# Kernel optimization log

Hardware: AMD Instinct MI355X
Metric: run time of the kernel (lower is better)

The kernel has to match this reference:

```python
import jax, jax.numpy as jnp
import numpy as np

B, H, W, C = 8, 112, 112, 128
NH, WS, SR, HIDDEN = 4, 7, 8, 512
EPS = 1e-5

def ln(x, g, b):
    mu = jnp.mean(x, axis=-1, keepdims=True)
    var = jnp.var(x, axis=-1, keepdims=True)
    return (x - mu) * jax.lax.rsqrt(var + EPS) * g + b

def local_attn(x, qkv_w, qkv_b, pw, pb):
    # windowed attention: (H,W) tiled into WSxWS windows, H%WS==W%WS==0 so no pad
    Bx, N, Cx = x.shape
    hd = Cx // NH
    _h, _w = H // WS, W // WS
    xw = x.reshape(Bx, _h, WS, _w, WS, Cx).transpose(0, 1, 3, 2, 4, 5)
    xw = xw.reshape(Bx, _h * _w, WS * WS, Cx)
    qkv = (xw @ qkv_w + qkv_b).reshape(Bx, _h * _w, WS * WS, 3, NH, hd)
    qkv = qkv.transpose(3, 0, 1, 4, 2, 5)  # 3, B, nW, NH, ws2, hd
    q, k, v = qkv[0], qkv[1], qkv[2]
    attn = jax.nn.softmax((q @ jnp.swapaxes(k, -2, -1)) * (hd ** -0.5), axis=-1)
    o = (attn @ v).transpose(0, 1, 3, 2, 4).reshape(Bx, _h, _w, WS, WS, Cx)
    o = o.transpose(0, 1, 3, 2, 4, 5).reshape(Bx, N, Cx)
    return o @ pw + pb

def global_attn(x, qw, qb, kvw, kvb, srw, srb, sng, snb, pw, pb):
    Bx, N, Cx = x.shape
    hd = Cx // NH
    q = (x @ qw + qb).reshape(Bx, N, NH, hd).transpose(0, 2, 1, 3)  # B,NH,N,hd
    xi = x.reshape(Bx, H, W, Cx)
    xs = jax.lax.conv_general_dilated(xi, srw, (SR, SR), 'VALID',
                                      dimension_numbers=('NHWC', 'HWIO', 'NHWC')) + srb
    xs = ln(xs.reshape(Bx, -1, Cx), sng, snb)  # B, M, C  (M = (H/SR)*(W/SR))
    kv = (xs @ kvw + kvb).reshape(Bx, -1, 2, NH, hd)
    k = kv[:, :, 0].transpose(0, 2, 1, 3)
    v = kv[:, :, 1].transpose(0, 2, 1, 3)
    attn = jax.nn.softmax(jnp.einsum('bhnd,bhmd->bhnm', q, k) * (hd ** -0.5), axis=-1)
    o = jnp.einsum('bhnm,bhmd->bhnd', attn, v).transpose(0, 2, 1, 3).reshape(Bx, N, Cx)
    return o @ pw + pb

def mlp(x, f1w, f1b, dww, dwb, f2w, f2b):
    h = x @ f1w + f1b
    hi = h.reshape(x.shape[0], H, W, HIDDEN)
    hi = jax.lax.conv_general_dilated(hi, dww, (1, 1), 'SAME',
                                      dimension_numbers=('NHWC', 'HWIO', 'NHWC'),
                                      feature_group_count=HIDDEN) + dwb
    h = jax.nn.gelu(hi.reshape(x.shape[0], -1, HIDDEN), approximate=False)
    return h @ f2w + f2b

def reference(x, l_n1_g, l_n1_b, l_qkv_w, l_qkv_b, l_pw, l_pb, l_n2_g, l_n2_b,
              l_f1w, l_f1b, l_dww, l_dwb, l_f2w, l_f2b,
              g_n1_g, g_n1_b, g_qw, g_qb, g_kvw, g_kvb, g_srw, g_srb, g_sng, g_snb,
              g_pw, g_pb, g_n2_g, g_n2_b, g_f1w, g_f1b, g_dww, g_dwb, g_f2w, g_f2b):
    # Local-attention Block
    x = x + local_attn(ln(x, l_n1_g, l_n1_b), l_qkv_w, l_qkv_b, l_pw, l_pb)
    x = x + mlp(ln(x, l_n2_g, l_n2_b), l_f1w, l_f1b, l_dww, l_dwb, l_f2w, l_f2b)
    # Global (spatial-reduction) attention Block
    x = x + global_attn(ln(x, g_n1_g, g_n1_b), g_qw, g_qb, g_kvw, g_kvb,
                        g_srw, g_srb, g_sng, g_snb, g_pw, g_pb)
    x = x + mlp(ln(x, g_n2_g, g_n2_b), g_f1w, g_f1b, g_dww, g_dwb, g_f2w, g_f2b)
    return x

def setup_inputs() -> dict:
    key = jax.random.key(0)
    cnt = [0]
    def rn(shp, s=0.02):
        cnt[0] += 1
        return (jax.random.normal(jax.random.fold_in(key, cnt[0]), shp, dtype=jnp.float32) * s)
    z = lambda shp: jnp.zeros(shp, jnp.float32)
    o = lambda shp: jnp.ones(shp, jnp.float32)
    return {
        'x': rn((B, H * W, C), 1.0),
        'l_n1_g': o((C,)), 'l_n1_b': z((C,)),
        'l_qkv_w': rn((C, 3 * C)), 'l_qkv_b': z((3 * C,)),
        'l_pw': rn((C, C)), 'l_pb': z((C,)),
        'l_n2_g': o((C,)), 'l_n2_b': z((C,)),
        'l_f1w': rn((C, HIDDEN)), 'l_f1b': z((HIDDEN,)),
        'l_dww': rn((3, 3, 1, HIDDEN), 0.1), 'l_dwb': z((HIDDEN,)),
        'l_f2w': rn((HIDDEN, C)), 'l_f2b': z((C,)),
        'g_n1_g': o((C,)), 'g_n1_b': z((C,)),
        'g_qw': rn((C, C)), 'g_qb': z((C,)),
        'g_kvw': rn((C, 2 * C)), 'g_kvb': z((2 * C,)),
        'g_srw': rn((SR, SR, C, C), 0.02), 'g_srb': z((C,)),
        'g_sng': o((C,)), 'g_snb': z((C,)),
        'g_pw': rn((C, C)), 'g_pb': z((C,)),
        'g_n2_g': o((C,)), 'g_n2_b': z((C,)),
        'g_f1w': rn((C, HIDDEN)), 'g_f1b': z((HIDDEN,)),
        'g_dww': rn((3, 3, 1, HIDDEN), 0.1), 'g_dwb': z((HIDDEN,)),
        'g_f2w': rn((HIDDEN, C)), 'g_f2b': z((C,)),
    }
```

## Files before the change

kernel.cpp:

```cpp
#include <hip/hip_runtime.h>
#include <hip/hip_bf16.h>

#define DI __device__ __forceinline__

typedef __attribute__((ext_vector_type(8))) __bf16 bf16x8;
typedef __attribute__((ext_vector_type(8))) short short8;
typedef __attribute__((ext_vector_type(4))) short short4v;
typedef __attribute__((ext_vector_type(4))) float f32x4;

DI short f2b(float f) {
    union { float f; unsigned u; } v; v.f = f;
    unsigned r = v.u + 0x7FFFu + ((v.u >> 16) & 1u);
    return (short)(r >> 16);
}
DI float b2f(short s) {
    union { unsigned u; float f; } v; v.u = ((unsigned)(unsigned short)s) << 16;
    return v.f;
}

DI void gll16(const short* g, short* l) {
    __builtin_amdgcn_global_load_lds(
        (const __attribute__((address_space(1))) void*)(g),
        (__attribute__((address_space(3))) void*)(l), 16, 0, 0);
}

DI float gelu(float a) {
    float z = fabsf(a) * 0.7071067811865475f;
    float t = __builtin_amdgcn_rcpf(fmaf(0.3275911f, z, 1.f));
    float p = t * fmaf(t, fmaf(t, fmaf(t, fmaf(t, 1.061405429f, -1.453152027f),
                                       1.421413741f), -0.284496736f), 0.254829592f);
    float e = __expf(-z * z);
    float er = fmaf(-p, e, 1.f);
    float sg = (a >= 0.f) ? er : -er;
    return 0.5f * a * (1.f + sg);
}

template<int OB, int HB, int HR, int LNO>
__global__ __launch_bounds__(256)
void gemm128(const short* __restrict__ A, int lda,
             const short* __restrict__ Wt, int ldw,
             const float* __restrict__ bias,
             void* __restrict__ Cv, int ldc,
             const float* __restrict__ R, int ldr,
             const float* __restrict__ lng, const float* __restrict__ lnb,
             short* __restrict__ lnout,
             int K)
{
    __shared__ short As[4096];
    __shared__ short Bs[4096];
    const int nx = gridDim.x;
    const int total = nx * gridDim.y;
    int bid = blockIdx.x + nx * blockIdx.y;
    if ((total & 7) == 0) bid = (bid & 7) * (total >> 3) + (bid >> 3);
    const int m0 = (bid / nx) * 128, n0 = (bid % nx) * 128;
    const int tid = threadIdx.x, lane = tid & 63, w = tid >> 6;
    const int wr = w >> 1, wc = w & 1;
    const int fr = lane & 15, fg = lane >> 4;

    const int i0 = tid, i1 = 256 + tid;
    const int r0 = i0 >> 2, p0 = i0 & 3;
    const int r1 = i1 >> 2, p1 = i1 & 3;
    const int s0 = (r0 & 3) ^ ((r0 >> 2) & 3);
    const int s1_ = (r1 & 3) ^ ((r1 >> 2) & 3);
    const short* aptr0 = A + (long long)(m0 + r0) * lda + (p0 ^ s0) * 8;
    const short* aptr1 = A + (long long)(m0 + r1) * lda + (p1 ^ s1_) * 8;
    const short* bptr0 = Wt + (long long)(n0 + r0) * ldw + (p0 ^ s0) * 8;
    const short* bptr1 = Wt + (long long)(n0 + r1) * ldw + (p1 ^ s1_) * 8;
    short* lA0 = As + w * 512;
    short* lA1 = As + 2048 + w * 512;
    short* lB0 = Bs + w * 512;
    short* lB1 = Bs + 2048 + w * 512;

    const int sf = (fr & 3) ^ ((fr >> 2) & 3);
    const short* pA = As + (wr * 64 + fr) * 32 + (fg ^ sf) * 8;
    const short* pB = Bs + (wc * 64 + fr) * 32 + (fg ^ sf) * 8;

    f32x4 zero = {0.f, 0.f, 0.f, 0.f};
    f32x4 acc[4][4];
    #pragma unroll
    for (int i = 0; i < 4; i++)
        #pragma unroll
        for (int j = 0; j < 4; j++) acc[i][j] = zero;

    for (int k0 = 0; k0 < K; k0 += 32) {
        __syncthreads();
        gll16(aptr0, lA0); gll16(aptr1, lA1);
        gll16(bptr0, lB0); gll16(bptr1, lB1);
        aptr0 += 32; aptr1 += 32; bptr0 += 32; bptr1 += 32;
        __syncthreads();
        bf16x8 af[4], bf[4];
        #pragma unroll
        for (int i = 0; i < 4; i++) af[i] = *(const bf16x8*)(pA + i * 512);
        #pragma unroll
        for (int j = 0; j < 4; j++) bf[j] = *(const bf16x8*)(pB + j * 512);
        #pragma unroll
        for (int i = 0; i < 4; i++)
            #pragma unroll
            for (int j = 0; j < 4; j++)
                acc[i][j] = __builtin_amdgcn_mfma_f32_16x16x32_bf16(bf[j], af[i], acc[i][j], 0, 0, 0);
    }

    const int mB = wr * 64 + fr;
    const int nB = wc * 64 + fg * 4;

    if (LNO) {
        float s1[4] = {0.f, 0.f, 0.f, 0.f}, s2[4] = {0.f, 0.f, 0.f, 0.f};
        #pragma unroll
        for (int mi = 0; mi < 4; mi++) {
            const long long m = m0 + mB + mi * 16;
            #pragma unroll
            for (int ni = 0; ni < 4; ni++) {
                const int n = nB + ni * 16;
                float4 bv = *(const float4*)&bias[n];
                float4 rv = *(const float4*)&R[m * ldr + n];
                const float* bvp = (const float*)&bv;
                const float* rvp = (const float*)&rv;
                #pragma unroll
                for (int v = 0; v < 4; v++) {
                    float val = acc[mi][ni][v] + bvp[v] + rvp[v];
                    acc[mi][ni][v] = val;
                    s1[mi] += val;
                    s2[mi] += val * val;
                }
                float4 st = {acc[mi][ni][0], acc[mi][ni][1], acc[mi][ni][2], acc[mi][ni][3]};
                *(float4*)&((float*)Cv)[m * ldc + n] = st;
            }
        }
        #pragma unroll
        for (int mi = 0; mi < 4; mi++) {
            s1[mi] += __shfl_xor(s1[mi], 16); s1[mi] += __shfl_xor(s1[mi], 32);
            s2[mi] += __shfl_xor(s2[mi], 16); s2[mi] += __shfl_xor(s2[mi], 32);
        }
        float* sc = (float*)As;
        __syncthreads();
        if (fg == 0) {
            #pragma unroll
            for (int mi = 0; mi < 4; mi++) {
                int rt = mB + mi * 16;
                sc[rt * 4 + wc * 2]     = s1[mi];
                sc[rt * 4 + wc * 2 + 1] = s2[mi];
            }
        }
        __syncthreads();
        #pragma unroll
        for (int mi = 0; mi < 4; mi++) {
            int rt = mB + mi * 16;
            long long m = m0 + rt;
            float t1 = sc[rt * 4] + sc[rt * 4 + 2];
            float t2 = sc[rt * 4 + 1] + sc[rt * 4 + 3];
            float mu = t1 * 0.0078125f;
            float var = t2 * 0.0078125f - mu * mu;
            float rs = rsqrtf(var + 1e-5f);
            #pragma unroll
            for (int ni = 0; ni < 4; ni++) {
                int n = nB + ni * 16;
                float4 gg = *(const float4*)&lng[n];
                float4 bb = *(const float4*)&lnb[n];
                const float* gp = (const float*)&gg;
                const float* bp = (const float*)&bb;
                short o[4];
                #pragma unroll
                for (int v = 0; v < 4; v++)
                    o[v] = f2b((acc[mi][ni][v] - mu) * rs * gp[v] + bp[v]);
                int2 pk;
                pk.x = ((int)(unsigned short)o[1] << 16) | (unsigned short)o[0];
                pk.y = ((int)(unsigned short)o[3] << 16) | (unsigned short)o[2];
                *(int2*)&lnout[m * 128 + n] = pk;
            }
        }
    } else {
        #pragma unroll
        for (int mi = 0; mi < 4; mi++) {
            const long long m = m0 + mB + mi * 16;
            #pragma unroll
            for (int ni = 0; ni < 4; ni++) {
                const int n = n0 + nB + ni * 16;
                float4 bv = {0.f, 0.f, 0.f, 0.f};
                float4 rv = {0.f, 0.f, 0.f, 0.f};
                if (HB) bv = *(const float4*)&bias[n];
                if (HR) rv = *(const float4*)&R[m * ldr + n];
                const float* bvp = (const float*)&bv;
                const float* rvp = (const float*)&rv;
                float val[4];
                #pragma unroll
                for (int v = 0; v < 4; v++)
                    val[v] = acc[mi][ni][v] + bvp[v] + rvp[v];
                if (OB) {
                    int2 pk;
                    pk.x = ((int)(unsigned short)f2b(val[1]) << 16) | (unsigned short)f2b(val[0]);
                    pk.y = ((int)(unsigned short)f2b(val[3]) << 16) | (unsigned short)f2b(val[2]);
                    *(int2*)&((short*)Cv)[m * ldc + n] = pk;
                } else {
                    float4 st = {val[0], val[1], val[2], val[3]};
                    *(float4*)&((float*)Cv)[m * ldc + n] = st;
                }
            }
        }
    }
}

template<int OB, int HB, int HR>
__global__ __launch_bounds__(256)
void gemm64(const short* __restrict__ A, int lda, long long sA,
            const short* __restrict__ Wt, int ldw, long long sW,
            const float* __restrict__ bias,
            void* __restrict__ Cv, int ldc, long long sC,
            const float* __restrict__ R, int ldr, long long sR,
            int M, int N, int K)
{
    __shared__ short As[2048];
    __shared__ short Bs[2048];
    const int z = blockIdx.z;
    A  += (long long)z * sA;
    Wt += (long long)z * sW;
    const int m0 = blockIdx.y * 64, n0 = blockIdx.x * 64;
    const int tid = threadIdx.x, lane = tid & 63, wv = tid >> 6;
    const int wr = wv >> 1, wc = wv & 1;
    const int lrow = tid >> 2, lch = tid & 3;
    const int wch = lch ^ (lrow & 3);

    f32x4 zero = {0.f, 0.f, 0.f, 0.f};
    f32x4 acc00 = zero, acc01 = zero, acc10 = zero, acc11 = zero;

    const short* arow = &A[(long long)(m0 + lrow) * lda + lch * 8];
    const short* brow = &Wt[(long long)(n0 + lrow) * ldw + lch * 8];
    short* asw = &As[lrow * 32 + wch * 8];
    short* bsw = &Bs[lrow * 32 + wch * 8];

    const int fr = lane & 15, fg = lane >> 4;
    const int c = ((fg ^ (fr & 3)) * 8);
    const int a0off = (wr * 32 + fr) * 32 + c;
    const int b0off = (wc * 32 + fr) * 32 + c;

    for (int k0 = 0; k0 < K; k0 += 32) {
        uint4 av = *(const uint4*)arow; arow += 32;
        uint4 bv = *(const uint4*)brow; brow += 32;
        __syncthreads();
        *(uint4*)asw = av;
        *(uint4*)bsw = bv;
        __syncthreads();
        bf16x8 a0 = *(const bf16x8*)&As[a0off];
        bf16x8 a1 = *(const bf16x8*)&As[a0off + 512];
        bf16x8 b0 = *(const bf16x8*)&Bs[b0off];
        bf16x8 b1 = *(const bf16x8*)&Bs[b0off + 512];
        acc00 = __builtin_amdgcn_mfma_f32_16x16x32_bf16(a0, b0, acc00, 0, 0, 0);
        acc01 = __builtin_amdgcn_mfma_f32_16x16x32_bf16(a0, b1, acc01, 0, 0, 0);
        acc10 = __builtin_amdgcn_mfma_f32_16x16x32_bf16(a1, b0, acc10, 0, 0, 0);
        acc11 = __builtin_amdgcn_mfma_f32_16x16x32_bf16(a1, b1, acc11, 0, 0, 0);
    }

    const long long cz = (long long)z * sC;
    const int rbase = m0 + wr * 32 + fg * 4;
    const int cbase = n0 + wc * 32 + fr;
    auto emit = [&](f32x4 a, int mi, int ni) {
        int cc = cbase + ni * 16;
        if (cc >= N) return;
        float bv = HB ? bias[cc] : 0.f;
        #pragma unroll
        for (int v = 0; v < 4; v++) {
            int rr = rbase + mi * 16 + v;
            if (rr >= M) continue;
            float val = a[v] + bv;
            if (HR) val += R[(long long)z * sR + (long long)rr * ldr + cc];
            if (OB) ((short*)Cv)[cz + (long long)rr * ldc + cc] = f2b(val);
            else    ((float*)Cv)[cz + (long long)rr * ldc + cc] = val;
        }
    };
    emit(acc00, 0, 0); emit(acc01, 0, 1); emit(acc10, 1, 0); emit(acc11, 1, 1);
}

__global__ __launch_bounds__(256)
void srgemm(const short* __restrict__ LNF, const short* __restrict__ Wt,
            float* __restrict__ PART)
{
    __shared__ short As[2048];
    __shared__ short Bs[2048];
    const int z = blockIdx.z;
    const int m0 = blockIdx.y * 64, n0 = blockIdx.x * 64;
    const int tid = threadIdx.x, lane = tid & 63, wv = tid >> 6;
    const int wr = wv >> 1, wc = wv & 1;
    const int lrow = tid >> 2, lch = tid & 3;
    const int wch = lch ^ (lrow & 3);

    f32x4 zero = {0.f, 0.f, 0.f, 0.f};
    f32x4 acc00 = zero, acc01 = zero, acc10 = zero, acc11 = zero;

    int row = m0 + lrow;
    int rc = row < 1568 ? row : 1567;
    int b = rc / 196, p = rc % 196;
    int oh = p / 14, ow = p % 14;
    int k0 = z * 256;
    int kh = k0 >> 10, koff = k0 & 1023;
    const short* arow = LNF + ((long long)(b * 12544 + (oh * 8 + kh) * 112 + ow * 8)) * 128
                        + koff + lch * 8;
    const short* brow = Wt + (long long)(n0 + lrow) * 8192 + k0 + lch * 8;
    short* asw = &As[lrow * 32 + wch * 8];
    short* bsw = &Bs[lrow * 32 + wch * 8];

    const int fr = lane & 15, fg = lane >> 4;
    const int c = ((fg ^ (fr & 3)) * 8);
    const int a0off = (wr * 32 + fr) * 32 + c;
    const int b0off = (wc * 32 + fr) * 32 + c;

    for (int kk = 0; kk < 256; kk += 32) {
        uint4 av = *(const uint4*)arow; arow += 32;
        uint4 bv = *(const uint4*)brow; brow += 32;
        __syncthreads();
        *(uint4*)asw = av;
        *(uint4*)bsw = bv;
        __syncthreads();
        bf16x8 a0 = *(const bf16x8*)&As[a0off];
        bf16x8 a1 = *(const bf16x8*)&As[a0off + 512];
        bf16x8 b0 = *(const bf16x8*)&Bs[b0off];
        bf16x8 b1 = *(const bf16x8*)&Bs[b0off + 512];
        acc00 = __builtin_amdgcn_mfma_f32_16x16x32_bf16(a0, b0, acc00, 0, 0, 0);
        acc01 = __builtin_amdgcn_mfma_f32_16x16x32_bf16(a0, b1, acc01, 0, 0, 0);
        acc10 = __builtin_amdgcn_mfma_f32_16x16x32_bf16(a1, b0, acc10, 0, 0, 0);
        acc11 = __builtin_amdgcn_mfma_f32_16x16x32_bf16(a1, b1, acc11, 0, 0, 0);
    }

    const int rbase = m0 + wr * 32 + fg * 4;
    const int cbase = n0 + wc * 32 + fr;
    auto emit = [&](f32x4 a, int mi, int ni) {
        int cc = cbase + ni * 16;
        #pragma unroll
        for (int v = 0; v < 4; v++) {
            int rr = rbase + mi * 16 + v;
            if (rr >= 1568) continue;
            PART[(long long)z * 200704 + (long long)rr * 128 + cc] = a[v];
        }
    };
    emit(acc00, 0, 0); emit(acc01, 0, 1); emit(acc10, 1, 0); emit(acc11, 1, 1);
}

__global__ void reduceXS(const float* __restrict__ PART, const float* __restrict__ bias,
                         float* __restrict__ XS)
{
    int i = blockIdx.x * 256 + threadIdx.x;
    float s = 0.f;
    #pragma unroll
    for (int z = 0; z < 32; z++) s += PART[(long long)z * 200704 + i];
    XS[i] = s + bias[i & 127];
}

__global__ __launch_bounds__(256)
void ln_kernel(const float* __restrict__ x, const float* __restrict__ g,
               const float* __restrict__ b, short* __restrict__ o, int rows)
{
    int row = blockIdx.x * 4 + (threadIdx.x >> 6);
    if (row >= rows) return;
    int lane = threadIdx.x & 63;
    const float2 v = *(const float2*)&x[(long long)row * 128 + lane * 2];
    float s = v.x + v.y;
    float ss = v.x * v.x + v.y * v.y;
    #pragma unroll
    for (int off = 1; off < 64; off <<= 1) {
        s += __shfl_xor(s, off);
        ss += __shfl_xor(ss, off);
    }
    float mu = s * 0.0078125f;
    float var = ss * 0.0078125f - mu * mu;
    float rs = rsqrtf(var + 1e-5f);
    float2 gg = *(const float2*)&g[lane * 2];
    float2 bb = *(const float2*)&b[lane * 2];
    short2 out;
    out.x = f2b((v.x - mu) * rs * gg.x + bb.x);
    out.y = f2b((v.y - mu) * rs * gg.y + bb.y);
    *(short2*)&o[(long long)row * 128 + lane * 2] = out;
}

__global__ void wtrans(const float* __restrict__ w, short* __restrict__ wt, int K, int N)
{
    long long idx = (long long)blockIdx.x * 256 + threadIdx.x;
    if (idx >= (long long)K * N) return;
    int k = (int)(idx / N), n = (int)(idx % N);
    wt[(long long)n * K + k] = f2b(w[idx]);
}

__global__ void packkv(const short* __restrict__ kvb, short* __restrict__ kp,
                       short* __restrict__ vt)
{
    int idx = blockIdx.x * 256 + threadIdx.x;
    if (idx >= 229376) return;
    int d = idx & 31;
    int m = (idx >> 5) % 224;
    int bh = idx / (224 * 32);
    int b = bh >> 2, h = bh & 3;
    short kv = 0, vv = 0;
    if (m < 196) {
        long long src = ((long long)b * 196 + m) * 256 + h * 32 + d;
        kv = kvb[src];
        vv = kvb[src + 128];
    }
    if (m < 208) kp[((long long)bh * 208 + m) * 32 + d] = kv;
    vt[((long long)bh * 32 + d) * 224 + m] = vv;
}

__global__ __launch_bounds__(512)
void lattn(const short* __restrict__ qkv, short* __restrict__ att)
{
    __shared__ short QKs[64 * 264];
    __shared__ short Vt[128 * 72];
    __shared__ short Pl[8 * 16 * 72];
    const int bi = blockIdx.x >> 8;
    const int win = blockIdx.x & 255;
    const int wy = win >> 4, wx = win & 15;
    const long long base = (long long)bi * 12544;
    const int tid = threadIdx.x;

    for (int i = tid; i < 1152; i += 512) {
        uint4 zz = {0, 0, 0, 0};
        *(uint4*)&Vt[i * 8] = zz;
    }
    __syncthreads();

    for (int idx = tid; idx < 2352; idx += 512) {
        int i = idx / 48, ch = idx % 48;
        long long n = base + (wy * 7 + i / 7) * 112 + wx * 7 + i % 7;
        uint4 v = *(const uint4*)&qkv[n * 384 + ch * 8];
        if (ch < 32) {
            *(uint4*)&QKs[i * 264 + ch * 8] = v;
        } else {
            int c0 = (ch - 32) * 8;
            const short* sp = (const short*)&v;
            #pragma unroll
            for (int u = 0; u < 8; u++) {
                int cc = c0 + u;
                Vt[cc * 72 + ((((i >> 3) ^ ((cc >> 3) & 7)) << 3) | (i & 7))] = sp[u];
            }
        }
    }
    __syncthreads();

    const int w = tid >> 6, l = tid & 63;
    const int h = w >> 1, qh = w & 1;
    const int q16 = l & 15, g = l >> 4;
    const float SC = 0.17677669529663689f;
    f32x4 zero = {0.f, 0.f, 0.f, 0.f};

    bf16x8 kf[4];
    #pragma unroll
    for (int kt = 0; kt < 4; kt++)
        kf[kt] = *(const bf16x8*)&QKs[(kt * 16 + q16) * 264 + 128 + h * 32 + g * 8];
    bf16x8 vf[2][2];
    #pragma unroll
    for (int dt = 0; dt < 2; dt++) {
        int cc = h * 32 + dt * 16 + q16;
        #pragma unroll
        for (int s2 = 0; s2 < 2; s2++)
            vf[dt][s2] = *(const bf16x8*)&Vt[cc * 72 + (((s2 * 4 + g) ^ ((cc >> 3) & 7)) << 3)];
    }
    short* pw = &Pl[(w * 16 + q16) * 72];

    for (int qt2 = 0; qt2 < 2; qt2++) {
        int qt = qh * 2 + qt2;
        bf16x8 qf = *(const bf16x8*)&QKs[(qt * 16 + q16) * 264 + h * 32 + g * 8];
        f32x4 s[4];
        #pragma unroll
        for (int kt = 0; kt < 4; kt++)
            s[kt] = __builtin_amdgcn_mfma_f32_16x16x32_bf16(kf[kt], qf, zero, 0, 0, 0);
        float mx = -1e30f;
        #pragma unroll
        for (int kt = 0; kt < 4; kt++) {
            #pragma unroll
            for (int v = 0; v < 4; v++) {
                int k = kt * 16 + g * 4 + v;
                if (k < 49) mx = fmaxf(mx, s[kt][v]);
            }
        }
        mx = fmaxf(mx, __shfl_xor(mx, 16));
        mx = fmaxf(mx, __shfl_xor(mx, 32));
        float sum = 0.f;
        #pragma unroll
        for (int kt = 0; kt < 4; kt++) {
            #pragma unroll
            for (int v = 0; v < 4; v++) {
                int k = kt * 16 + g * 4 + v;
                float p = (k < 49) ? __expf(SC * (s[kt][v] - mx)) : 0.f;
                s[kt][v] = p;
                sum += p;
            }
        }
        sum += __shfl_xor(sum, 16);
        sum += __shfl_xor(sum, 32);
        float inv = 1.f / sum;
        #pragma unroll
        for (int kt = 0; kt < 4; kt++) {
            int lo = ((int)(unsigned short)f2b(s[kt][1] * inv) << 16) | (unsigned short)f2b(s[kt][0] * inv);
            int hi = ((int)(unsigned short)f2b(s[kt][3] * inv) << 16) | (unsigned short)f2b(s[kt][2] * inv);
            int2 pr; pr.x = lo; pr.y = hi;
            *(int2*)&pw[kt * 16 + g * 4] = pr;
        }
        f32x4 o0 = zero, o1 = zero;
        #pragma unroll
        for (int s2 = 0; s2 < 2; s2++) {
            bf16x8 pa = *(const bf16x8*)&pw[s2 * 32 + g * 8];
            o0 = __builtin_amdgcn_mfma_f32_16x16x32_bf16(pa, vf[0][s2], o0, 0, 0, 0);
            o1 = __builtin_amdgcn_mfma_f32_16x16x32_bf16(pa, vf[1][s2], o1, 0, 0, 0);
        }
        #pragma unroll
        for (int v = 0; v < 4; v++) {
            int q = qt * 16 + g * 4 + v;
            if (q < 49) {
                long long n = base + (wy * 7 + q / 7) * 112 + wx * 7 + q % 7;
                att[n * 128 + h * 32 + q16]      = f2b(o0[v]);
                att[n * 128 + h * 32 + 16 + q16] = f2b(o1[v]);
            }
        }
    }
}

__global__ __launch_bounds__(256)
void gattn(const short* __restrict__ Q, const short* __restrict__ KP,
           const short* __restrict__ VT, short* __restrict__ O)
{
    __shared__ short Ks[208 * 40];
    __shared__ short Vt[32 * 232];
    __shared__ short Pl[4 * 16 * 232];
    const int qb = blockIdx.x;
    const int bh = blockIdx.y;
    const int b = bh >> 2, h = bh & 3;
    const int tid = threadIdx.x, w = tid >> 6, l = tid & 63;
    const int q16 = l & 15, g = l >> 4;

    for (int idx = tid; idx < 832; idx += 256) {
        int m = idx >> 2, dg = idx & 3;
        uint4 v = *(const uint4*)&KP[((long long)bh * 208 + m) * 32 + dg * 8];
        *(uint4*)&Ks[m * 40 + ((dg ^ (m & 3)) * 8)] = v;
    }
    for (int idx = tid; idx < 896; idx += 256) {
        int d = idx / 28, mg = idx % 28;
        uint4 v = *(const uint4*)&VT[((long long)bh * 32 + d) * 224 + mg * 8];
        *(uint4*)&Vt[d * 232 + mg * 8] = v;
    }
    const long long qbase = (long long)b * 12544 + qb * 128 + w * 32;
    bf16x8 qfa = *(const bf16x8*)&Q[(qbase + q16) * 128 + h * 32 + g * 8];
    bf16x8 qfb = *(const bf16x8*)&Q[(qbase + 16 + q16) * 128 + h * 32 + g * 8];
    __syncthreads();

    const float SC = 0.17677669529663689f;
    f32x4 zero = {0.f, 0.f, 0.f, 0.f};
    short* pw = &Pl[(w * 16 + q16) * 232];
    const int xk = (g ^ (q16 & 3)) * 8;

    #pragma unroll
    for (int qt = 0; qt < 2; qt++) {
        bf16x8 qf = qt ? qfb : qfa;
        f32x4 s[13];
        #pragma unroll
        for (int t = 0; t < 13; t++) {
            bf16x8 a = *(const bf16x8*)&Ks[(t * 16 + q16) * 40 + xk];
            s[t] = __builtin_amdgcn_mfma_f32_16x16x32_bf16(a, qf, zero, 0, 0, 0);
        }
        float mx = -1e30f;
        #pragma unroll
        for (int t = 0; t < 13; t++) {
            #pragma unroll
            for (int v = 0; v < 4; v++) {
                int k = t * 16 + g * 4 + v;
                if (k < 196) mx = fmaxf(mx, s[t][v]);
            }
        }
        mx = fmaxf(mx, __shfl_xor(mx, 16));
        mx = fmaxf(mx, __shfl_xor(mx, 32));
        float sum = 0.f;
        #pragma unroll
        for (int t = 0; t < 13; t++) {
            #pragma unroll
            for (int v = 0; v < 4; v++) {
                int k = t * 16 + g * 4 + v;
                float pv = (k < 196) ? __expf(SC * (s[t][v] - mx)) : 0.f;
                s[t][v] = pv;
                sum += pv;
            }
        }
        sum += __shfl_xor(sum, 16);
        sum += __shfl_xor(sum, 32);
        float inv = 1.f / sum;
        #pragma unroll
        for (int t = 0; t < 13; t++) {
            int lo = ((int)(unsigned short)f2b(s[t][1] * inv) << 16) | (unsigned short)f2b(s[t][0] * inv);
            int hi = ((int)(unsigned short)f2b(s[t][3] * inv) << 16) | (unsigned short)f2b(s[t][2] * inv);
            int2 pr; pr.x = lo; pr.y = hi;
            *(int2*)&pw[t * 16 + g * 4] = pr;
        }
        int2 zz; zz.x = 0; zz.y = 0;
        *(int2*)&pw[208 + g * 4] = zz;

        f32x4 o0 = zero, o1 = zero;
        #pragma unroll
        for (int kc = 0; kc < 7; kc++) {
            bf16x8 pa = *(const bf16x8*)&pw[kc * 32 + g * 8];
            bf16x8 v0 = *(const bf16x8*)&Vt[q16 * 232 + kc * 32 + g * 8];
            bf16x8 v1 = *(const bf16x8*)&Vt[(16 + q16) * 232 + kc * 32 + g * 8];
            o0 = __builtin_amdgcn_mfma_f32_16x16x32_bf16(v0, pa, o0, 0, 0, 0);
            o1 = __builtin_amdgcn_mfma_f32_16x16x32_bf16(v1, pa, o1, 0, 0, 0);
        }
        const long long r = qbase + qt * 16 + q16;
        int2 p0, p1;
        p0.x = ((int)(unsigned short)f2b(o0[1]) << 16) | (unsigned short)f2b(o0[0]);
        p0.y = ((int)(unsigned short)f2b(o0[3]) << 16) | (unsigned short)f2b(o0[2]);
        p1.x = ((int)(unsigned short)f2b(o1[1]) << 16) | (unsigned short)f2b(o1[0]);
        p1.y = ((int)(unsigned short)f2b(o1[3]) << 16) | (unsigned short)f2b(o1[2]);
        *(int2*)&O[r * 128 + h * 32 + g * 4]      = p0;
        *(int2*)&O[r * 128 + h * 32 + 16 + g * 4] = p1;
    }
}

__global__ __launch_bounds__(256)
void dwgelu(const short* __restrict__ h1, const float* __restrict__ w,
            const float* __restrict__ bias, short* __restrict__ h2)
{
    int bid = blockIdx.x;
    bid = (bid & 7) * (gridDim.x >> 3) + (bid >> 3);
    const int idx = bid * 256 + threadIdx.x;
    const int cg = idx & 127;
    const int rem = idx >> 7;
    const int img = rem / 1568;
    const int t = rem % 1568;
    const int x0 = (t % 56) * 2;
    const int y0 = (t / 56) * 4;
    const int c0 = cg << 2;

    float wreg[9][4];
    #pragma unroll
    for (int tp = 0; tp < 9; tp++) {
        float4 v = *(const float4*)&w[tp * 512 + c0];
        wreg[tp][0] = v.x; wreg[tp][1] = v.y; wreg[tp][2] = v.z; wreg[tp][3] = v.w;
    }
    float4 bv = *(const float4*)&bias[c0];
    float acc[4][2][4];
    #pragma unroll
    for (int r = 0; r < 4; r++)
        #pragma unroll
        for (int oc = 0; oc < 2; oc++) {
            acc[r][oc][0] = bv.x; acc[r][oc][1] = bv.y;
            acc[r][oc][2] = bv.z; acc[r][oc][3] = bv.w;
        }
    const long long ibase = (long long)img * 12544;

    #pragma unroll
    for (int dy = -1; dy <= 4; dy++) {
        const int yy = y0 + dy;
        const bool rowok = (unsigned)yy < 112u;
        float rowf[4][4];
        #pragma unroll
        for (int kx = 0; kx < 4; kx++) {
            const int xx = x0 - 1 + kx;
            short4v sv = {0, 0, 0, 0};
            if (rowok && (unsigned)xx < 112u)
                sv = *(const short4v*)&h1[(ibase + yy * 112 + xx) * 512 + c0];
            #pragma unroll
            for (int u = 0; u < 4; u++) rowf[kx][u] = b2f(sv[u]);
        }
        #pragma unroll
        for (int ky = 0; ky < 3; ky++) {
            const int r = dy + 1 - ky;
            if (r < 0 || r > 3) continue;
            #pragma unroll
            for (int oc = 0; oc < 2; oc++)
                #pragma unroll
                for (int kx = 0; kx < 3; kx++)
                    #pragma unroll
                    for (int u = 0; u < 4; u++)
                        acc[r][oc][u] = fmaf(rowf[oc + kx][u], wreg[ky * 3 + kx][u], acc[r][oc][u]);
        }
    }
    #pragma unroll
    for (int r = 0; r < 4; r++)
        #pragma unroll
        for (int oc = 0; oc < 2; oc++) {
            short o[4];
            #pragma unroll
            for (int u = 0; u < 4; u++) o[u] = f2b(gelu(acc[r][oc][u]));
            int2 pk;
            pk.x = ((int)(unsigned short)o[1] << 16) | (unsigned short)o[0];
            pk.y = ((int)(unsigned short)o[3] << 16) | (unsigned short)o[2];
            *(int2*)&h2[(ibase + (y0 + r) * 112 + x0 + oc) * 512 + c0] = pk;
        }
}

extern "C" void kernel_launch(void* const* d_in, const int* in_sizes, int n_in,
                              void* d_out, int out_size, void* d_ws, size_t ws_size,
                              hipStream_t stream)
{
    (void)in_sizes; (void)n_in; (void)out_size;
    const float* X      = (const float*)d_in[0];
    const float* l_n1_g = (const float*)d_in[1];
    const float* l_n1_b = (const float*)d_in[2];
    const float* l_qkv_w= (const float*)d_in[3];
    const float* l_qkv_b= (const float*)d_in[4];
    const float* l_pw   = (const float*)d_in[5];
    const float* l_pb   = (const float*)d_in[6];
    const float* l_n2_g = (const float*)d_in[7];
    const float* l_n2_b = (const float*)d_in[8];
    const float* l_f1w  = (const float*)d_in[9];
    const float* l_f1b  = (const float*)d_in[10];
    const float* l_dww  = (const float*)d_in[11];
    const float* l_dwb  = (const float*)d_in[12];
    const float* l_f2w  = (const float*)d_in[13];
    const float* l_f2b  = (const float*)d_in[14];
    const float* g_n1_g = (const float*)d_in[15];
    const float* g_n1_b = (const float*)d_in[16];
    const float* g_qw   = (const float*)d_in[17];
    const float* g_qb   = (const float*)d_in[18];
    const float* g_kvw  = (const float*)d_in[19];
    const float* g_kvb  = (const float*)d_in[20];
    const float* g_srw  = (const float*)d_in[21];
    const float* g_srb  = (const float*)d_in[22];
    const float* g_sng  = (const float*)d_in[23];
    const float* g_snb  = (const float*)d_in[24];
    const float* g_pw   = (const float*)d_in[25];
    const float* g_pb   = (const float*)d_in[26];
    const float* g_n2_g = (const float*)d_in[27];
    const float* g_n2_b = (const float*)d_in[28];
    const float* g_f2w  = (const float*)d_in[33];
    const float* g_f2b  = (const float*)d_in[34];
    const float* g_f1w  = (const float*)d_in[29];
    const float* g_f1b  = (const float*)d_in[30];
    const float* g_dww  = (const float*)d_in[31];
    const float* g_dwb  = (const float*)d_in[32];

    const long long NPB = 12544;
    const long long BN  = 100352;
    const int iBN = (int)BN;

    float* OUT = (float*)d_out;
    char* ws = (char*)d_ws;
    size_t off = 0;
    auto alloc = [&](size_t bytes) { size_t o = off; off += (bytes + 255) & ~(size_t)255; return o; };
    short* WT_QKV = (short*)(ws + alloc(384 * 128 * 2));
    short* WT_LPW = (short*)(ws + alloc(128 * 128 * 2));
    short* WT_LF1 = (short*)(ws + alloc(512 * 128 * 2));
    short* WT_LF2 = (short*)(ws + alloc(128 * 512 * 2));
    short* WT_GQ  = (short*)(ws + alloc(128 * 128 * 2));
    short* WT_GKV = (short*)(ws + alloc(256 * 128 * 2));
    short* WT_GSR = (short*)(ws + alloc(128 * 8192 * 2));
    short* WT_GPW = (short*)(ws + alloc(128 * 128 * 2));
    short* WT_GF1 = (short*)(ws + alloc(512 * 128 * 2));
    short* WT_GF2 = (short*)(ws + alloc(128 * 512 * 2));
    short* LNF    = (short*)(ws + alloc((size_t)BN * 128 * 2));
    char*  U      = ws + alloc(0);

    const size_t SZ_H1   = (size_t)BN * 512 * 2;
    const bool big = ws_size >= off + 2 * SZ_H1 + 4096;
    short* QKVB = (short*)(U + 0);
    short* ATT  = (short*)(U + 77070336);
    float* PART = (float*)(U + 0);
    float* XS   = (float*)(U + 25690368);
    short* XSLN = (short*)(U + 26493184);
    short* KVB  = (short*)(U + 26894592);
    short* QBUF = (short*)(U + 27697408);
    short* KP   = (short*)(U + 53387776);
    short* VT   = (short*)(U + 53387776 + 425984);

    wtrans<<<192, 256, 0, stream>>>(l_qkv_w, WT_QKV, 128, 384);
    wtrans<<<64, 256, 0, stream>>>(l_pw, WT_LPW, 128, 128);
    wtrans<<<256, 256, 0, stream>>>(l_f1w, WT_LF1, 128, 512);
    wtrans<<<256, 256, 0, stream>>>(l_f2w, WT_LF2, 512, 128);
    wtrans<<<64, 256, 0, stream>>>(g_qw, WT_GQ, 128, 128);
    wtrans<<<128, 256, 0, stream>>>(g_kvw, WT_GKV, 128, 256);
    wtrans<<<4096, 256, 0, stream>>>(g_srw, WT_GSR, 8192, 128);
    wtrans<<<64, 256, 0, stream>>>(g_pw, WT_GPW, 128, 128);
    wtrans<<<256, 256, 0, stream>>>(g_f1w, WT_GF1, 128, 512);
    wtrans<<<256, 256, 0, stream>>>(g_f2w, WT_GF2, 512, 128);

    const int CB = big ? 8 : 2;
    short* H1 = (short*)(U + 0);

    ln_kernel<<<25088, 256, 0, stream>>>(X, l_n1_g, l_n1_b, LNF, iBN);
    gemm128<1, 1, 0, 0><<<dim3(3, 784), 256, 0, stream>>>(
        LNF, 128, WT_QKV, 128, l_qkv_b, QKVB, 384, nullptr, 0,
        nullptr, nullptr, nullptr, 128);
    lattn<<<2048, 512, 0, stream>>>(QKVB, ATT);
    gemm128<0, 1, 1, 1><<<dim3(1, 784), 256, 0, stream>>>(
        ATT, 128, WT_LPW, 128, l_pb, OUT, 128, X, 128,
        l_n2_g, l_n2_b, LNF, 128);

    {
        short* H2 = (short*)(U + (size_t)CB * NPB * 512 * 2);
        for (int b0 = 0; b0 < 8; b0 += CB) {
            int Mc = CB * 12544;
            gemm128<1, 1, 0, 0><<<dim3(4, Mc / 128), 256, 0, stream>>>(
                LNF + (long long)b0 * NPB * 128, 128, WT_LF1, 128, l_f1b,
                H1, 512, nullptr, 0, nullptr, nullptr, nullptr, 128);
            dwgelu<<<CB * 784, 256, 0, stream>>>(H1, l_dww, l_dwb, H2);
            gemm128<0, 1, 1, 1><<<dim3(1, Mc / 128), 256, 0, stream>>>(
                H2, 512, WT_LF2, 512, l_f2b,
                OUT + (long long)b0 * NPB * 128, 128,
                OUT + (long long)b0 * NPB * 128, 128,
                g_n1_g, g_n1_b, LNF + (long long)b0 * NPB * 128, 512);
        }
    }

    gemm128<1, 1, 0, 0><<<dim3(1, 784), 256, 0, stream>>>(
        LNF, 128, WT_GQ, 128, g_qb, QBUF, 128, nullptr, 0,
        nullptr, nullptr, nullptr, 128);
    srgemm<<<dim3(2, 25, 32), 256, 0, stream>>>(LNF, WT_GSR, PART);
    reduceXS<<<784, 256, 0, stream>>>(PART, g_srb, XS);
    ln_kernel<<<392, 256, 0, stream>>>(XS, g_sng, g_snb, XSLN, 1568);
    gemm64<1, 1, 0><<<dim3(4, 25, 1), 256, 0, stream>>>(
        XSLN, 128, 0, WT_GKV, 128, 0, g_kvb,
        KVB, 256, 0, nullptr, 0, 0, 1568, 256, 128);
    packkv<<<896, 256, 0, stream>>>(KVB, KP, VT);
    gattn<<<dim3(98, 32), 256, 0, stream>>>(QBUF, KP, VT, ATT);
    gemm128<0, 1, 1, 1><<<dim3(1, 784), 256, 0, stream>>>(
        ATT, 128, WT_GPW, 128, g_pb, OUT, 128, OUT, 128,
        g_n2_g, g_n2_b, LNF, 128);

    {
        short* H2 = (short*)(U + (size_t)CB * NPB * 512 * 2);
        for (int b0 = 0; b0 < 8; b0 += CB) {
            int Mc = CB * 12544;
            gemm128<1, 1, 0, 0><<<dim3(4, Mc / 128), 256, 0, stream>>>(
                LNF + (long long)b0 * NPB * 128, 128, WT_GF1, 128, g_f1b,
                H1, 512, nullptr, 0, nullptr, nullptr, nullptr, 128);
            dwgelu<<<CB * 784, 256, 0, stream>>>(H1, g_dww, g_dwb, H2);
            gemm128<0, 1, 1, 0><<<dim3(1, Mc / 128), 256, 0, stream>>>(
                H2, 512, WT_GF2, 512, g_f2b,
                OUT + (long long)b0 * NPB * 128, 128,
                OUT + (long long)b0 * NPB * 128, 128,
                nullptr, nullptr, nullptr, 512);
        }
    }
}
```

Before: 631.3 us.

## Store residual stream in bf16, prefetch residual before GEMM loop, fast-path dwconv interior

The residual stream between blocks moves from fp32 OUT to a new bf16 RES buffer. A new ln_first kernel writes it, and the LN-fused GEMM epilogues read and write bf16, which roughly halves residual read/write traffic. Residual loads are now issued before the K loop so their latency overlaps with the MFMA work. The depthwise conv gains a branch-free interior path that skips bounds checks. The cost is rounding the residual to bf16 at every block, which may hurt accuracy, plus extra registers held for the prefetched residual.

```diff
diff --git a/kernel.cpp b/kernel.cpp
--- a/kernel.cpp
+++ b/kernel.cpp
@@ -16,6 +16,12 @@
 DI float b2f(short s) {
     union { unsigned u; float f; } v; v.u = ((unsigned)(unsigned short)s) << 16;
     return v.f;
+}
+DI float lo16(int x) {
+    union { unsigned u; float f; } v; v.u = (unsigned)x << 16; return v.f;
+}
+DI float hi16(int x) {
+    union { unsigned u; float f; } v; v.u = (unsigned)x & 0xffff0000u; return v.f;
 }
 
 DI void gll16(const short* g, short* l) {
@@ -41,7 +47,7 @@
              const short* __restrict__ Wt, int ldw,
              const float* __restrict__ bias,
              void* __restrict__ Cv, int ldc,
-             const float* __restrict__ R, int ldr,
+             const short* __restrict__ R, int ldr,
              const float* __restrict__ lng, const float* __restrict__ lnb,
              short* __restrict__ lnout,
              int K)
@@ -56,6 +62,8 @@
     const int tid = threadIdx.x, lane = tid & 63, w = tid >> 6;
     const int wr = w >> 1, wc = w & 1;
     const int fr = lane & 15, fg = lane >> 4;
+    const int mB = wr * 64 + fr;
+    const int nB = wc * 64 + fg * 4;
 
     const int i0 = tid, i1 = 256 + tid;
     const int r0 = i0 >> 2, p0 = i0 & 3;
@@ -75,6 +83,17 @@
     const short* pA = As + (wr * 64 + fr) * 32 + (fg ^ sf) * 8;
     const short* pB = Bs + (wc * 64 + fr) * 32 + (fg ^ sf) * 8;
 
+    int2 rpre[4][4];
+    if (HR) {
+        #pragma unroll
+        for (int mi = 0; mi < 4; mi++) {
+            const long long m = m0 + mB + mi * 16;
+            #pragma unroll
+            for (int ni = 0; ni < 4; ni++)
+                rpre[mi][ni] = *(const int2*)&R[m * ldr + n0 + nB + ni * 16];
+        }
+    }
+
     f32x4 zero = {0.f, 0.f, 0.f, 0.f};
     f32x4 acc[4][4];
     #pragma unroll
@@ -100,9 +119,6 @@
                 acc[i][j] = __builtin_amdgcn_mfma_f32_16x16x32_bf16(bf[j], af[i], acc[i][j], 0, 0, 0);
     }
 
-    const int mB = wr * 64 + fr;
-    const int nB = wc * 64 + fg * 4;
-
     if (LNO) {
         float s1[4] = {0.f, 0.f, 0.f, 0.f}, s2[4] = {0.f, 0.f, 0.f, 0.f};
         #pragma unroll
@@ -112,18 +128,20 @@
             for (int ni = 0; ni < 4; ni++) {
                 const int n = nB + ni * 16;
                 float4 bv = *(const float4*)&bias[n];
-                float4 rv = *(const float4*)&R[m * ldr + n];
                 const float* bvp = (const float*)&bv;
-                const float* rvp = (const float*)&rv;
+                float rv[4] = {lo16(rpre[mi][ni].x), hi16(rpre[mi][ni].x),
+                               lo16(rpre[mi][ni].y), hi16(rpre[mi][ni].y)};
                 #pragma unroll
                 for (int v = 0; v < 4; v++) {
-                    float val = acc[mi][ni][v] + bvp[v] + rvp[v];
+                    float val = acc[mi][ni][v] + bvp[v] + rv[v];
                     acc[mi][ni][v] = val;
                     s1[mi] += val;
                     s2[mi] += val * val;
                 }
-                float4 st = {acc[mi][ni][0], acc[mi][ni][1], acc[mi][ni][2], acc[mi][ni][3]};
-                *(float4*)&((float*)Cv)[m * ldc + n] = st;
+                int2 pk;
+                pk.x = ((int)(unsigned short)f2b(acc[mi][ni][1]) << 16) | (unsigned short)f2b(acc[mi][ni][0]);
+                pk.y = ((int)(unsigned short)f2b(acc[mi][ni][3]) << 16) | (unsigned short)f2b(acc[mi][ni][2]);
+                *(int2*)&((short*)Cv)[m * ldc + n] = pk;
             }
         }
         #pragma unroll
@@ -176,15 +194,17 @@
             for (int ni = 0; ni < 4; ni++) {
                 const int n = n0 + nB + ni * 16;
                 float4 bv = {0.f, 0.f, 0.f, 0.f};
-                float4 rv = {0.f, 0.f, 0.f, 0.f};
                 if (HB) bv = *(const float4*)&bias[n];
-                if (HR) rv = *(const float4*)&R[m * ldr + n];
                 const float* bvp = (const float*)&bv;
-                const float* rvp = (const float*)&rv;
+                float rv[4] = {0.f, 0.f, 0.f, 0.f};
+                if (HR) {
+                    rv[0] = lo16(rpre[mi][ni].x); rv[1] = hi16(rpre[mi][ni].x);
+                    rv[2] = lo16(rpre[mi][ni].y); rv[3] = hi16(rpre[mi][ni].y);
+                }
                 float val[4];
                 #pragma unroll
                 for (int v = 0; v < 4; v++)
-                    val[v] = acc[mi][ni][v] + bvp[v] + rvp[v];
+                    val[v] = acc[mi][ni][v] + bvp[v] + rv[v];
                 if (OB) {
                     int2 pk;
                     pk.x = ((int)(unsigned short)f2b(val[1]) << 16) | (unsigned short)f2b(val[0]);
@@ -199,13 +219,12 @@
     }
 }
 
-template<int OB, int HB, int HR>
+template<int OB, int HB>
 __global__ __launch_bounds__(256)
 void gemm64(const short* __restrict__ A, int lda, long long sA,
             const short* __restrict__ Wt, int ldw, long long sW,
             const float* __restrict__ bias,
             void* __restrict__ Cv, int ldc, long long sC,
-            const float* __restrict__ R, int ldr, long long sR,
             int M, int N, int K)
 {
     __shared__ short As[2048];
@@ -261,7 +280,6 @@
             int rr = rbase + mi * 16 + v;
             if (rr >= M) continue;
             float val = a[v] + bv;
-            if (HR) val += R[(long long)z * sR + (long long)rr * ldr + cc];
             if (OB) ((short*)Cv)[cz + (long long)rr * ldc + cc] = f2b(val);
             else    ((float*)Cv)[cz + (long long)rr * ldc + cc] = val;
         }
@@ -369,6 +387,35 @@
     *(short2*)&o[(long long)row * 128 + lane * 2] = out;
 }
 
+__global__ __launch_bounds__(256)
+void ln_first(const float* __restrict__ x, const float* __restrict__ g,
+              const float* __restrict__ b, short* __restrict__ o,
+              short* __restrict__ res)
+{
+    int row = blockIdx.x * 4 + (threadIdx.x >> 6);
+    int lane = threadIdx.x & 63;
+    const float2 v = *(const float2*)&x[(long long)row * 128 + lane * 2];
+    short2 rc;
+    rc.x = f2b(v.x); rc.y = f2b(v.y);
+    *(short2*)&res[(long long)row * 128 + lane * 2] = rc;
+    float s = v.x + v.y;
+    float ss = v.x * v.x + v.y * v.y;
+    #pragma unroll
+    for (int off = 1; off < 64; off <<= 1) {
+        s += __shfl_xor(s, off);
+        ss += __shfl_xor(ss, off);
+    }
+    float mu = s * 0.0078125f;
+    float var = ss * 0.0078125f - mu * mu;
+    float rs = rsqrtf(var + 1e-5f);
+    float2 gg = *(const float2*)&g[lane * 2];
+    float2 bb = *(const float2*)&b[lane * 2];
+    short2 out;
+    out.x = f2b((v.x - mu) * rs * gg.x + bb.x);
+    out.y = f2b((v.y - mu) * rs * gg.y + bb.y);
+    *(short2*)&o[(long long)row * 128 + lane * 2] = out;
+}
+
 __global__ void wtrans(const float* __restrict__ w, short* __restrict__ wt, int K, int N)
 {
     long long idx = (long long)blockIdx.x * 256 + threadIdx.x;
@@ -639,31 +686,57 @@
         }
     const long long ibase = (long long)img * 12544;
 
-    #pragma unroll
-    for (int dy = -1; dy <= 4; dy++) {
-        const int yy = y0 + dy;
-        const bool rowok = (unsigned)yy < 112u;
-        float rowf[4][4];
-        #pragma unroll
-        for (int kx = 0; kx < 4; kx++) {
-            const int xx = x0 - 1 + kx;
-            short4v sv = {0, 0, 0, 0};
-            if (rowok && (unsigned)xx < 112u)
-                sv = *(const short4v*)&h1[(ibase + yy * 112 + xx) * 512 + c0];
-            #pragma unroll
-            for (int u = 0; u < 4; u++) rowf[kx][u] = b2f(sv[u]);
-        }
-        #pragma unroll
-        for (int ky = 0; ky < 3; ky++) {
-            const int r = dy + 1 - ky;
-            if (r < 0 || r > 3) continue;
-            #pragma unroll
-            for (int oc = 0; oc < 2; oc++)
+    if (x0 >= 1 && x0 <= 109 && y0 >= 1 && y0 <= 107) {
+        const short* base = &h1[(ibase + (long long)(y0 - 1) * 112 + (x0 - 1)) * 512 + c0];
+        #pragma unroll
+        for (int dy = 0; dy < 6; dy++) {
+            float rowf[4][4];
+            #pragma unroll
+            for (int kx = 0; kx < 4; kx++) {
+                short4v sv = *(const short4v*)&base[((long long)dy * 112 + kx) * 512];
                 #pragma unroll
-                for (int kx = 0; kx < 3; kx++)
+                for (int u = 0; u < 4; u++) rowf[kx][u] = b2f(sv[u]);
+            }
+            #pragma unroll
+            for (int ky = 0; ky < 3; ky++) {
+                const int r = dy - ky;
+                if (r < 0 || r > 3) continue;
+                #pragma unroll
+                for (int oc = 0; oc < 2; oc++)
                     #pragma unroll
-                    for (int u = 0; u < 4; u++)
-                        acc[r][oc][u] = fmaf(rowf[oc + kx][u], wreg[ky * 3 + kx][u], acc[r][oc][u]);
+                    for (int kx = 0; kx < 3; kx++)
+                        #pragma unroll
+                        for (int u = 0; u < 4; u++)
+                            acc[r][oc][u] = fmaf(rowf[oc + kx][u], wreg[ky * 3 + kx][u], acc[r][oc][u]);
+            }
+        }
+    } else {
+        #pragma unroll
+        for (int dy = -1; dy <= 4; dy++) {
+            const int yy = y0 + dy;
+            const bool rowok = (unsigned)yy < 112u;
+            float rowf[4][4];
+            #pragma unroll
+            for (int kx = 0; kx < 4; kx++) {
+                const int xx = x0 - 1 + kx;
+                short4v sv = {0, 0, 0, 0};
+                if (rowok && (unsigned)xx < 112u)
+                    sv = *(const short4v*)&h1[(ibase + yy * 112 + xx) * 512 + c0];
+                #pragma unroll
+                for (int u = 0; u < 4; u++) rowf[kx][u] = b2f(sv[u]);
+            }
+            #pragma unroll
+            for (int ky = 0; ky < 3; ky++) {
+                const int r = dy + 1 - ky;
+                if (r < 0 || r > 3) continue;
+                #pragma unroll
+                for (int oc = 0; oc < 2; oc++)
+                    #pragma unroll
+                    for (int kx = 0; kx < 3; kx++)
+                        #pragma unroll
+                        for (int u = 0; u < 4; u++)
+                            acc[r][oc][u] = fmaf(rowf[oc + kx][u], wreg[ky * 3 + kx][u], acc[r][oc][u]);
+            }
         }
     }
     #pragma unroll
@@ -714,12 +787,12 @@
     const float* g_pb   = (const float*)d_in[26];
     const float* g_n2_g = (const float*)d_in[27];
     const float* g_n2_b = (const float*)d_in[28];
-    const float* g_f2w  = (const float*)d_in[33];
-    const float* g_f2b  = (const float*)d_in[34];
     const float* g_f1w  = (const float*)d_in[29];
     const float* g_f1b  = (const float*)d_in[30];
     const float* g_dww  = (const float*)d_in[31];
     const float* g_dwb  = (const float*)d_in[32];
+    const float* g_f2w  = (const float*)d_in[33];
+    const float* g_f2b  = (const float*)d_in[34];
 
     const long long NPB = 12544;
     const long long BN  = 100352;
@@ -740,6 +813,7 @@
     short* WT_GF1 = (short*)(ws + alloc(512 * 128 * 2));
     short* WT_GF2 = (short*)(ws + alloc(128 * 512 * 2));
     short* LNF    = (short*)(ws + alloc((size_t)BN * 128 * 2));
+    short* RES    = (short*)(ws + alloc((size_t)BN * 128 * 2));
     char*  U      = ws + alloc(0);
 
     const size_t SZ_H1   = (size_t)BN * 512 * 2;
@@ -768,13 +842,13 @@
     const int CB = big ? 8 : 2;
     short* H1 = (short*)(U + 0);
 
-    ln_kernel<<<25088, 256, 0, stream>>>(X, l_n1_g, l_n1_b, LNF, iBN);
+    ln_first<<<25088, 256, 0, stream>>>(X, l_n1_g, l_n1_b, LNF, RES);
     gemm128<1, 1, 0, 0><<<dim3(3, 784), 256, 0, stream>>>(
         LNF, 128, WT_QKV, 128, l_qkv_b, QKVB, 384, nullptr, 0,
         nullptr, nullptr, nullptr, 128);
     lattn<<<2048, 512, 0, stream>>>(QKVB, ATT);
-    gemm128<0, 1, 1, 1><<<dim3(1, 784), 256, 0, stream>>>(
-        ATT, 128, WT_LPW, 128, l_pb, OUT, 128, X, 128,
+    gemm128<1, 1, 1, 1><<<dim3(1, 784), 256, 0, stream>>>(
+        ATT, 128, WT_LPW, 128, l_pb, RES, 128, RES, 128,
         l_n2_g, l_n2_b, LNF, 128);
 
     {
@@ -785,10 +859,10 @@
                 LNF + (long long)b0 * NPB * 128, 128, WT_LF1, 128, l_f1b,
                 H1, 512, nullptr, 0, nullptr, nullptr, nullptr, 128);
             dwgelu<<<CB * 784, 256, 0, stream>>>(H1, l_dww, l_dwb, H2);
-            gemm128<0, 1, 1, 1><<<dim3(1, Mc / 128), 256, 0, stream>>>(
+            gemm128<1, 1, 1, 1><<<dim3(1, Mc / 128), 256, 0, stream>>>(
                 H2, 512, WT_LF2, 512, l_f2b,
-                OUT + (long long)b0 * NPB * 128, 128,
-                OUT + (long long)b0 * NPB * 128, 128,
+                RES + (long long)b0 * NPB * 128, 128,
+                RES + (long long)b0 * NPB * 128, 128,
                 g_n1_g, g_n1_b, LNF + (long long)b0 * NPB * 128, 512);
         }
     }
@@ -799,13 +873,13 @@
     srgemm<<<dim3(2, 25, 32), 256, 0, stream>>>(LNF, WT_GSR, PART);
     reduceXS<<<784, 256, 0, stream>>>(PART, g_srb, XS);
     ln_kernel<<<392, 256, 0, stream>>>(XS, g_sng, g_snb, XSLN, 1568);
-    gemm64<1, 1, 0><<<dim3(4, 25, 1), 256, 0, stream>>>(
+    gemm64<1, 1><<<dim3(4, 25, 1), 256, 0, stream>>>(
         XSLN, 128, 0, WT_GKV, 128, 0, g_kvb,
-        KVB, 256, 0, nullptr, 0, 0, 1568, 256, 128);
+        KVB, 256, 0, 1568, 256, 128);
     packkv<<<896, 256, 0, stream>>>(KVB, KP, VT);
     gattn<<<dim3(98, 32), 256, 0, stream>>>(QBUF, KP, VT, ATT);
-    gemm128<0, 1, 1, 1><<<dim3(1, 784), 256, 0, stream>>>(
-        ATT, 128, WT_GPW, 128, g_pb, OUT, 128, OUT, 128,
+    gemm128<1, 1, 1, 1><<<dim3(1, 784), 256, 0, stream>>>(
+        ATT, 128, WT_GPW, 128, g_pb, RES, 128, RES, 128,
         g_n2_g, g_n2_b, LNF, 128);
 
     {
@@ -819,7 +893,7 @@
             gemm128<0, 1, 1, 0><<<dim3(1, Mc / 128), 256, 0, stream>>>(
                 H2, 512, WT_GF2, 512, g_f2b,
                 OUT + (long long)b0 * NPB * 128, 128,
-                OUT + (long long)b0 * NPB * 128, 128,
+                RES + (long long)b0 * NPB * 128, 128,
                 nullptr, nullptr, nullptr, 512);
         }
     }
```

New measurement: 581.7 us. 7.9% less time.
